# Kernel optimization log

Measured on AMD Instinct MI355X. Metric: run time of the kernel, lower is better.

Reference implementation:

```python
import jax, jax.numpy as jnp
import numpy as np

NUM_TOKENS = 2048
HIDDEN = 1024
INTER = 2048
NUM_EXPERTS = 8
TOPK = 2


def setup_inputs() -> dict:
    key = jax.random.key(0)
    k1, k2, k3, k4 = jax.random.split(key, 4)
    hidden_states = jax.random.normal(k1, (NUM_TOKENS, HIDDEN), dtype=jnp.float32)
    router_logits = jax.random.normal(k2, (NUM_TOKENS, NUM_EXPERTS), dtype=jnp.float32)
    # fc1: [E, hidden, 2*intermediate] (proj/gate for SwiGLU), fc2: [E, intermediate, hidden]
    w1 = jax.random.normal(k3, (NUM_EXPERTS, HIDDEN, 2 * INTER), dtype=jnp.float32) * 0.02
    w2 = jax.random.normal(k4, (NUM_EXPERTS, INTER, HIDDEN), dtype=jnp.float32) * 0.02
    return {"hidden_states": hidden_states, "router_logits": router_logits, "w1": w1, "w2": w2}


def _grouped_gemm(x, w, expert_ids):
    """x: [T, D], w: [E, D, O], expert_ids: [T] -> [T, O].
    Tokens are routed to expert expert_ids[t]; equivalent to the sequential
    per-expert GEMM on contiguously sorted tokens. Small fixed loop over E."""
    out = jnp.zeros((x.shape[0], w.shape[-1]), dtype=x.dtype)
    for e in range(w.shape[0]):
        mask = (expert_ids == e)[:, None]
        out = out + jnp.where(mask, x, 0.0) @ w[e]
    return out


def reference(hidden_states, router_logits, w1, w2):
    # top-k routing + softmax over the selected logits
    top_logits, top_idx = jax.lax.top_k(router_logits, TOPK)      # [N, K]
    scores = jax.nn.softmax(top_logits, axis=-1)                  # [N, K]

    flat_idx = top_idx.reshape(-1)                                # [N*K]
    sorted_indices = jnp.argsort(flat_idx)                        # permute tokens grouped by expert
    permuted = hidden_states[sorted_indices // TOPK]              # [N*K, D]
    sorted_experts = flat_idx[sorted_indices]                     # [N*K] expert id per permuted row

    fc1_out = _grouped_gemm(permuted, w1, sorted_experts)         # [N*K, 2*I]
    proj, gate = jnp.split(fc1_out, 2, axis=-1)
    act = jax.nn.silu(proj) * gate                                # SwiGLU
    expert_out = _grouped_gemm(act, w2, sorted_experts)           # [N*K, D]

    # unpermute (scatter back) and weighted combine over top-k
    unpermuted = jnp.zeros_like(expert_out).at[sorted_indices].set(expert_out)
    unpermuted = unpermuted.reshape(-1, TOPK, expert_out.shape[-1])
    return (unpermuted * scores[..., None]).sum(axis=1)           # [N, D]
```

## Files before the change

kernel.cpp:

```cpp
#include <hip/hip_runtime.h>
#include <hip/hip_bf16.h>

constexpr int T = 2048;
constexpr int H = 1024;
constexpr int I = 2048;
constexpr int N2 = 2 * I;
constexpr int RCAP = 5120;
constexpr int MAXT = 40;

constexpr int WS_OFF = 16;
constexpr int WS_TEXP = 32;
constexpr int WS_TOPKP = 4256;
constexpr int WS_ROWTOK = 8352;
constexpr int WS_TOKROW = 13472;
constexpr size_t WSB_ZROW = 114688;
constexpr size_t WSB_HSB  = 131072;
constexpr size_t WSB_ACT  = 8u << 20;
constexpr size_t WSB_PW1  = 32u << 20;
constexpr size_t WSB_PW2  = 96u << 20;

constexpr int PW1_BLKS = 8192;
constexpr int PW2_BLKS = 4096;
constexpr int HSB_BLKS = T * H / 2048;
constexpr int FC1_BLKS = 32 * MAXT;

typedef __attribute__((ext_vector_type(4))) float f32x4;
typedef __attribute__((ext_vector_type(8))) short s16x8;

__device__ __forceinline__ short f2bf(float f) {
    unsigned u = __float_as_uint(f);
    u += 0x7FFFu + ((u >> 16) & 1u);
    return (short)(u >> 16);
}

#define MFMA16(a, b, c) __builtin_amdgcn_mfma_f32_16x16x32_bf16(a, b, c, 0, 0, 0)

__device__ __forceinline__ void gl2lds16(const void* g, void* l) {
    __builtin_amdgcn_global_load_lds(
        (const __attribute__((address_space(1))) void*)g,
        (__attribute__((address_space(3))) void*)l, 16, 0, 0);
}

__global__ __launch_bounds__(256) void routing_kernel(const float* __restrict__ logits,
                                                      int* __restrict__ wsi,
                                                      float* __restrict__ wsf) {
    __shared__ int cnt[8], base[9], fill[8];
    const int t = threadIdx.x;
    if (t < 8) { cnt[t] = 0; fill[t] = 0; }
    for (int r = t; r < RCAP; r += 256) wsi[WS_ROWTOK + r] = -1;
    unsigned short* zr = (unsigned short*)((char*)wsi + WSB_ZROW);
    for (int i = t; i < H; i += 256) zr[i] = 0;
    __syncthreads();

    int e0a[8], e1a[8];
    #pragma unroll
    for (int j = 0; j < 8; j++) {
        int tok = t * 8 + j;
        const float* l = logits + tok * 8;
        float v0 = -1e30f; int i0 = 0;
        #pragma unroll
        for (int i = 0; i < 8; i++) { float v = l[i]; if (v > v0) { v0 = v; i0 = i; } }
        float v1 = -1e30f; int i1 = 0;
        #pragma unroll
        for (int i = 0; i < 8; i++) { if (i == i0) continue; float v = l[i]; if (v > v1) { v1 = v; i1 = i; } }
        float ex = __expf(v1 - v0);
        float inv = 1.f / (1.f + ex);
        wsf[WS_TOPKP + tok * 2] = inv;
        wsf[WS_TOPKP + tok * 2 + 1] = ex * inv;
        e0a[j] = i0; e1a[j] = i1;
        atomicAdd(&cnt[i0], 1);
        atomicAdd(&cnt[i1], 1);
    }
    __syncthreads();
    if (t == 0) {
        int acc = 0;
        for (int e = 0; e < 8; e++) { base[e] = acc; acc += (cnt[e] + 127) & ~127; }
        base[8] = acc;
        for (int e = 0; e < 9; e++) wsi[WS_OFF + e] = base[e];
    }
    __syncthreads();
    for (int tt = t; tt < MAXT; tt += 256) {
        int rb = tt * 128, ex = 0;
        for (int e = 0; e < 8; e++)
            if (rb >= base[e] && rb < base[e + 1]) ex = e;
        wsi[WS_TEXP + tt] = ex;
    }
    #pragma unroll
    for (int j = 0; j < 8; j++) {
        int tok = t * 8 + j;
        int ee[2] = {e0a[j], e1a[j]};
        #pragma unroll
        for (int k = 0; k < 2; k++) {
            int e = ee[k];
            int slot = atomicAdd(&fill[e], 1);
            int r = base[e] + slot;
            wsi[WS_ROWTOK + r] = tok;
            wsi[WS_TOKROW + tok * 2 + k] = r;
        }
    }
}

__global__ __launch_bounds__(256) void prep_kernel(
    const float* __restrict__ w1, unsigned short* __restrict__ pw1,
    const float* __restrict__ w2, unsigned short* __restrict__ pw2,
    const float* __restrict__ hs, unsigned short* __restrict__ hsb) {
    const int t = threadIdx.x;
    if (blockIdx.x < PW1_BLKS) {
        int b = blockIdx.x;
        int k0i = b & 31, ct = (b >> 5) & 31, e = b >> 10;
        const float* src = w1 + (size_t)e * H * N2;
        unsigned short* dst = pw1 + (size_t)b * 4096;
        #pragma unroll
        for (int j = 0; j < 2; j++) {
            int g = t + j * 256;
            int kg = g >> 7, n = g & 127;
            int sub = n >> 5, within = n & 31;
            int col = ((sub & 1) ? I : 0) + ct * 64 + (sub >> 1) * 32 + within;
            int kbase = k0i * 32 + kg * 8;
            const float* sp = src + (size_t)kbase * N2 + col;
            s16x8 s;
            #pragma unroll
            for (int kk = 0; kk < 8; kk++) s[kk] = f2bf(sp[(size_t)kk * N2]);
            *(s16x8*)(dst + g * 8) = s;
        }
    } else if (blockIdx.x < PW1_BLKS + PW2_BLKS) {
        int b = blockIdx.x - PW1_BLKS;
        int k0i = b & 63, ht = (b >> 6) & 7, e = b >> 9;
        const float* src = w2 + (size_t)e * I * H;
        unsigned short* dst = pw2 + (size_t)b * 4096;
        #pragma unroll
        for (int j = 0; j < 2; j++) {
            int g = t + j * 256;
            int kg = g >> 7, n = g & 127;
            int col = ht * 128 + n;
            int kbase = k0i * 32 + kg * 8;
            const float* sp = src + (size_t)kbase * H + col;
            s16x8 s;
            #pragma unroll
            for (int kk = 0; kk < 8; kk++) s[kk] = f2bf(sp[(size_t)kk * H]);
            *(s16x8*)(dst + g * 8) = s;
        }
    } else {
        int i = ((blockIdx.x - PW1_BLKS - PW2_BLKS) * 256 + t) * 8;
        f32x4 a = *(const f32x4*)(hs + i);
        f32x4 b = *(const f32x4*)(hs + i + 4);
        s16x8 s = {f2bf(a[0]), f2bf(a[1]), f2bf(a[2]), f2bf(a[3]),
                   f2bf(b[0]), f2bf(b[1]), f2bf(b[2]), f2bf(b[3])};
        *(s16x8*)(hsb + i) = s;
    }
}

__global__ __launch_bounds__(256, 2) void fc1_kernel(
    const unsigned short* __restrict__ hsb, const unsigned short* __restrict__ pw1,
    const int* __restrict__ wsi, const unsigned short* __restrict__ zrow,
    unsigned short* __restrict__ act) {
    __shared__ __align__(16) unsigned short Al[512 * 8];
    __shared__ __align__(16) unsigned short Bl[512 * 8];
    const int t = threadIdx.x;
    const int ct = blockIdx.x & 31, rt = blockIdx.x >> 5;
    const int rowb = rt * 128;
    if (rowb >= wsi[WS_OFF + 8]) return;
    const int e = wsi[WS_TEXP + rt];
    const unsigned short* pb = pw1 + (size_t)((e * 32 + ct) * 32) * 4096;

    const int m = t & 127;
    const int tok = wsi[WS_ROWTOK + rowb + m];
    const unsigned short* rp = (tok >= 0) ? (hsb + (size_t)tok * H) : zrow;
    const int kga = t >> 7;

    const int lane = t & 63, w = t >> 6, wr = w >> 1, wc = w & 1;
    const int q = lane >> 4, l16 = lane & 15;

    f32x4 zero = {0.f, 0.f, 0.f, 0.f};
    f32x4 acc[4][4];
    #pragma unroll
    for (int mi = 0; mi < 4; mi++)
        #pragma unroll
        for (int ni = 0; ni < 4; ni++) acc[mi][ni] = zero;

    for (int k0i = 0; k0i < 32; k0i++) {
        const int k0 = k0i * 32;
        gl2lds16(rp + k0 + kga * 8, &Al[t * 8]);
        gl2lds16(rp + k0 + (kga + 2) * 8, &Al[(t + 256) * 8]);
        const unsigned short* ps = pb + (size_t)k0i * 4096;
        gl2lds16(ps + t * 8, &Bl[t * 8]);
        gl2lds16(ps + (t + 256) * 8, &Bl[(t + 256) * 8]);
        __syncthreads();

        s16x8 af[4], bf[4];
        #pragma unroll
        for (int mi = 0; mi < 4; mi++)
            af[mi] = *(const s16x8*)&Al[(q * 128 + wr * 64 + mi * 16 + l16) * 8];
        #pragma unroll
        for (int ni = 0; ni < 4; ni++)
            bf[ni] = *(const s16x8*)&Bl[(q * 128 + wc * 64 + ni * 16 + l16) * 8];
        #pragma unroll
        for (int mi = 0; mi < 4; mi++)
            #pragma unroll
            for (int ni = 0; ni < 4; ni++)
                acc[mi][ni] = MFMA16(af[mi], bf[ni], acc[mi][ni]);
        __syncthreads();
    }

    #pragma unroll
    for (int mi = 0; mi < 4; mi++)
        #pragma unroll
        for (int r = 0; r < 4; r++) {
            int row = rowb + wr * 64 + mi * 16 + q * 4 + r;
            #pragma unroll
            for (int ni = 0; ni < 2; ni++) {
                int col = ct * 64 + wc * 32 + ni * 16 + l16;
                float p = acc[mi][ni][r], g = acc[mi][ni + 2][r];
                float val = p * g / (1.f + __expf(-p));
                act[(size_t)row * I + col] = (unsigned short)f2bf(val);
            }
        }
}

__global__ __launch_bounds__(256, 2) void fc2_kernel(
    const unsigned short* __restrict__ act, const unsigned short* __restrict__ pw2,
    const int* __restrict__ wsi, float* __restrict__ eo) {
    __shared__ __align__(16) unsigned short Al[512 * 8];
    __shared__ __align__(16) unsigned short Bl[512 * 8];
    const int t = threadIdx.x;
    const int ht = blockIdx.x, rt = blockIdx.y, ks = blockIdx.z;
    const int rowb = rt * 128;
    if (rowb >= wsi[WS_OFF + 8]) return;
    const int e = wsi[WS_TEXP + rt];
    const unsigned short* pb = pw2 + (size_t)((e * 8 + ht) * 64) * 4096;

    const int m = t & 127;
    const unsigned short* rp = act + (size_t)(rowb + m) * I;
    const int kga = t >> 7;

    const int lane = t & 63, w = t >> 6, wr = w >> 1, wc = w & 1;
    const int q = lane >> 4, l16 = lane & 15;

    f32x4 zero = {0.f, 0.f, 0.f, 0.f};
    f32x4 acc[4][4];
    #pragma unroll
    for (int mi = 0; mi < 4; mi++)
        #pragma unroll
        for (int ni = 0; ni < 4; ni++) acc[mi][ni] = zero;

    for (int k0i = ks * 32; k0i < ks * 32 + 32; k0i++) {
        const int k0 = k0i * 32;
        gl2lds16(rp + k0 + kga * 8, &Al[t * 8]);
        gl2lds16(rp + k0 + (kga + 2) * 8, &Al[(t + 256) * 8]);
        const unsigned short* ps = pb + (size_t)k0i * 4096;
        gl2lds16(ps + t * 8, &Bl[t * 8]);
        gl2lds16(ps + (t + 256) * 8, &Bl[(t + 256) * 8]);
        __syncthreads();

        s16x8 af[4], bf[4];
        #pragma unroll
        for (int mi = 0; mi < 4; mi++)
            af[mi] = *(const s16x8*)&Al[(q * 128 + wr * 64 + mi * 16 + l16) * 8];
        #pragma unroll
        for (int ni = 0; ni < 4; ni++)
            bf[ni] = *(const s16x8*)&Bl[(q * 128 + wc * 64 + ni * 16 + l16) * 8];
        #pragma unroll
        for (int mi = 0; mi < 4; mi++)
            #pragma unroll
            for (int ni = 0; ni < 4; ni++)
                acc[mi][ni] = MFMA16(af[mi], bf[ni], acc[mi][ni]);
        __syncthreads();
    }

    float* ed = eo + (size_t)ks * RCAP * H;
    #pragma unroll
    for (int mi = 0; mi < 4; mi++)
        #pragma unroll
        for (int r = 0; r < 4; r++) {
            int row = rowb + wr * 64 + mi * 16 + q * 4 + r;
            #pragma unroll
            for (int ni = 0; ni < 4; ni++) {
                int col = ht * 128 + wc * 64 + ni * 16 + l16;
                ed[(size_t)row * H + col] = acc[mi][ni][r];
            }
        }
}

__global__ __launch_bounds__(256) void combine_kernel(
    const float* __restrict__ eo, const int* __restrict__ wsi,
    const float* __restrict__ wsf, float* __restrict__ out) {
    const int tok = blockIdx.x;
    const int r0 = wsi[WS_TOKROW + tok * 2], r1 = wsi[WS_TOKROW + tok * 2 + 1];
    const float s0 = wsf[WS_TOPKP + tok * 2], s1 = wsf[WS_TOPKP + tok * 2 + 1];
    const float* a0 = eo + (size_t)r0 * H;
    const float* a1 = eo + (size_t)RCAP * H + (size_t)r0 * H;
    const float* b0 = eo + (size_t)r1 * H;
    const float* b1 = eo + (size_t)RCAP * H + (size_t)r1 * H;
    const int c = threadIdx.x * 4;
    f32x4 va0 = *(const f32x4*)(a0 + c), va1 = *(const f32x4*)(a1 + c);
    f32x4 vb0 = *(const f32x4*)(b0 + c), vb1 = *(const f32x4*)(b1 + c);
    f32x4 r;
    #pragma unroll
    for (int i = 0; i < 4; i++) r[i] = s0 * (va0[i] + va1[i]) + s1 * (vb0[i] + vb1[i]);
    *(f32x4*)(out + (size_t)tok * H + c) = r;
}

extern "C" void kernel_launch(void* const* d_in, const int* in_sizes, int n_in,
                              void* d_out, int out_size, void* d_ws, size_t ws_size,
                              hipStream_t stream) {
    const float* hs     = (const float*)d_in[0];
    const float* logits = (const float*)d_in[1];
    const float* w1     = (const float*)d_in[2];
    const float* w2     = (const float*)d_in[3];
    float* out = (float*)d_out;
    int* wsi = (int*)d_ws;
    float* wsf = (float*)d_ws;
    unsigned short* zrow = (unsigned short*)((char*)d_ws + WSB_ZROW);
    unsigned short* hsb  = (unsigned short*)((char*)d_ws + WSB_HSB);
    unsigned short* act  = (unsigned short*)((char*)d_ws + WSB_ACT);
    unsigned short* pw1  = (unsigned short*)((char*)d_ws + WSB_PW1);
    unsigned short* pw2  = (unsigned short*)((char*)d_ws + WSB_PW2);
    float* eo = (float*)((char*)d_ws + WSB_PW1);

    routing_kernel<<<1, 256, 0, stream>>>(logits, wsi, wsf);
    prep_kernel<<<PW1_BLKS + PW2_BLKS + HSB_BLKS, 256, 0, stream>>>(w1, pw1, w2, pw2, hs, hsb);
    fc1_kernel<<<FC1_BLKS, 256, 0, stream>>>(hsb, pw1, wsi, zrow, act);
    fc2_kernel<<<dim3(8, MAXT, 2), 256, 0, stream>>>(act, pw2, wsi, eo);
    combine_kernel<<<T, 256, 0, stream>>>(eo, wsi, wsf, out);
}
```

Baseline: 381.8 us.

## Stage weight repack through LDS with coalesced vector loads

The bf16 weight-packing prep kernel now reads 32-row by 512-column fp32 tiles with contiguous 16-byte vector loads, converts them into shared memory, then gathers the k-strided 8-element groups from LDS to write the packed layout. The old code loaded eight scalars strided by a full row per output vector, which gave poorly coalesced global reads over a large weight set. Blocks become fewer and larger, and the change adds a 32KB LDS buffer, a barrier, and possible LDS bank conflicts on the strided gathers.

```diff
diff --git a/kernel.cpp b/kernel.cpp
--- a/kernel.cpp
+++ b/kernel.cpp
@@ -19,8 +19,8 @@
 constexpr size_t WSB_PW1  = 32u << 20;
 constexpr size_t WSB_PW2  = 96u << 20;
 
-constexpr int PW1_BLKS = 8192;
-constexpr int PW2_BLKS = 4096;
+constexpr int W1T_BLKS = 8 * 32 * 8;
+constexpr int W2T_BLKS = 8 * 64 * 2;
 constexpr int HSB_BLKS = T * H / 2048;
 constexpr int FC1_BLKS = 32 * MAXT;
 
@@ -104,44 +104,70 @@
     const float* __restrict__ w1, unsigned short* __restrict__ pw1,
     const float* __restrict__ w2, unsigned short* __restrict__ pw2,
     const float* __restrict__ hs, unsigned short* __restrict__ hsb) {
+    __shared__ __align__(16) unsigned short L[32 * 512];
     const int t = threadIdx.x;
-    if (blockIdx.x < PW1_BLKS) {
+    if (blockIdx.x < W1T_BLKS) {
         int b = blockIdx.x;
-        int k0i = b & 31, ct = (b >> 5) & 31, e = b >> 10;
-        const float* src = w1 + (size_t)e * H * N2;
-        unsigned short* dst = pw1 + (size_t)b * 4096;
-        #pragma unroll
-        for (int j = 0; j < 2; j++) {
-            int g = t + j * 256;
-            int kg = g >> 7, n = g & 127;
-            int sub = n >> 5, within = n & 31;
-            int col = ((sub & 1) ? I : 0) + ct * 64 + (sub >> 1) * 32 + within;
-            int kbase = k0i * 32 + kg * 8;
-            const float* sp = src + (size_t)kbase * N2 + col;
+        int cs = b & 7, k0i = (b >> 3) & 31, e = b >> 8;
+        const float* src = w1 + (size_t)e * H * N2 + (size_t)(k0i * 32) * N2 + cs * 512;
+        #pragma unroll
+        for (int i = 0; i < 8; i++) {
+            int c = t + i * 256;
+            int row = c >> 6, col8 = (c & 63) * 8;
+            const float* sp = src + (size_t)row * N2 + col8;
+            f32x4 a = *(const f32x4*)sp;
+            f32x4 bb = *(const f32x4*)(sp + 4);
+            s16x8 s = {f2bf(a[0]), f2bf(a[1]), f2bf(a[2]), f2bf(a[3]),
+                       f2bf(bb[0]), f2bf(bb[1]), f2bf(bb[2]), f2bf(bb[3])};
+            *(s16x8*)&L[c * 8] = s;
+        }
+        __syncthreads();
+        int gate = cs >> 2;
+        int ctbase = (cs & 3) * 8;
+        unsigned short* dstb = pw1 + (size_t)(e * 1024 + k0i) * 4096;
+        #pragma unroll
+        for (int i = 0; i < 8; i++) {
+            int cidx = t + i * 256;
+            int within = cidx & 31, nhalf = (cidx >> 5) & 1;
+            int kg = (cidx >> 6) & 3, ctp = cidx >> 8;
+            int x = ctp * 64 + nhalf * 32 + within;
+            int n = gate * 32 + nhalf * 64 + within;
             s16x8 s;
             #pragma unroll
-            for (int kk = 0; kk < 8; kk++) s[kk] = f2bf(sp[(size_t)kk * N2]);
-            *(s16x8*)(dst + g * 8) = s;
-        }
-    } else if (blockIdx.x < PW1_BLKS + PW2_BLKS) {
-        int b = blockIdx.x - PW1_BLKS;
-        int k0i = b & 63, ht = (b >> 6) & 7, e = b >> 9;
-        const float* src = w2 + (size_t)e * I * H;
-        unsigned short* dst = pw2 + (size_t)b * 4096;
-        #pragma unroll
-        for (int j = 0; j < 2; j++) {
-            int g = t + j * 256;
-            int kg = g >> 7, n = g & 127;
-            int col = ht * 128 + n;
-            int kbase = k0i * 32 + kg * 8;
-            const float* sp = src + (size_t)kbase * H + col;
+            for (int kk = 0; kk < 8; kk++) s[kk] = (short)L[(kg * 8 + kk) * 512 + x];
+            int ct = ctbase + ctp;
+            *(s16x8*)(dstb + (size_t)ct * 32 * 4096 + (kg * 128 + n) * 8) = s;
+        }
+    } else if (blockIdx.x < W1T_BLKS + W2T_BLKS) {
+        int b = blockIdx.x - W1T_BLKS;
+        int cs = b & 1, k0i = (b >> 1) & 63, e = b >> 7;
+        const float* src = w2 + (size_t)e * I * H + (size_t)(k0i * 32) * H + cs * 512;
+        #pragma unroll
+        for (int i = 0; i < 8; i++) {
+            int c = t + i * 256;
+            int row = c >> 6, col8 = (c & 63) * 8;
+            const float* sp = src + (size_t)row * H + col8;
+            f32x4 a = *(const f32x4*)sp;
+            f32x4 bb = *(const f32x4*)(sp + 4);
+            s16x8 s = {f2bf(a[0]), f2bf(a[1]), f2bf(a[2]), f2bf(a[3]),
+                       f2bf(bb[0]), f2bf(bb[1]), f2bf(bb[2]), f2bf(bb[3])};
+            *(s16x8*)&L[c * 8] = s;
+        }
+        __syncthreads();
+        unsigned short* dstb = pw2 + (size_t)(e * 512 + k0i) * 4096;
+        #pragma unroll
+        for (int i = 0; i < 8; i++) {
+            int cidx = t + i * 256;
+            int n = cidx & 127, kg = (cidx >> 7) & 3, htp = cidx >> 9;
+            int x = htp * 128 + n;
             s16x8 s;
             #pragma unroll
-            for (int kk = 0; kk < 8; kk++) s[kk] = f2bf(sp[(size_t)kk * H]);
-            *(s16x8*)(dst + g * 8) = s;
+            for (int kk = 0; kk < 8; kk++) s[kk] = (short)L[(kg * 8 + kk) * 512 + x];
+            int ht = cs * 4 + htp;
+            *(s16x8*)(dstb + (size_t)ht * 64 * 4096 + (kg * 128 + n) * 8) = s;
         }
     } else {
-        int i = ((blockIdx.x - PW1_BLKS - PW2_BLKS) * 256 + t) * 8;
+        int i = ((blockIdx.x - W1T_BLKS - W2T_BLKS) * 256 + t) * 8;
         f32x4 a = *(const f32x4*)(hs + i);
         f32x4 b = *(const f32x4*)(hs + i + 4);
         s16x8 s = {f2bf(a[0]), f2bf(a[1]), f2bf(a[2]), f2bf(a[3]),
@@ -318,7 +344,7 @@
     float* eo = (float*)((char*)d_ws + WSB_PW1);
 
     routing_kernel<<<1, 256, 0, stream>>>(logits, wsi, wsf);
-    prep_kernel<<<PW1_BLKS + PW2_BLKS + HSB_BLKS, 256, 0, stream>>>(w1, pw1, w2, pw2, hs, hsb);
+    prep_kernel<<<W1T_BLKS + W2T_BLKS + HSB_BLKS, 256, 0, stream>>>(w1, pw1, w2, pw2, hs, hsb);
     fc1_kernel<<<FC1_BLKS, 256, 0, stream>>>(hsb, pw1, wsi, zrow, act);
     fc2_kernel<<<dim3(8, MAXT, 2), 256, 0, stream>>>(act, pw2, wsi, eo);
     combine_kernel<<<T, 256, 0, stream>>>(eo, wsi, wsf, out);
```

Measured after the change: 382.8 us. Within noise of the previous version (+0.3%).
